# Optimization experiments

Measured on AMD Instinct MI355X. Metric: run time of the kernel, lower is better.

The kernel has to match this reference:

```python
import jax, jax.numpy as jnp
import numpy as np

EPS = 1e-06

def _l2_norm(t):
    # normalize over channel dim (-2): einsum('bcn,bn->bcn', t, 1/||t||_{2,dim=-2})
    inv = 1.0 / jnp.linalg.norm(t, ord=2, axis=-2)  # (B, L)
    return t * inv[:, None, :]


def setup_inputs() -> dict:
    key = jax.random.key(0)
    ks = jax.random.split(key, 8)
    B, C, D = 16, 2048, 1024  # D == d_model == Length
    s = 1.0 / np.sqrt(D)
    return {
        "x": jax.random.normal(ks[0], (B, C, D), dtype=jnp.float32),
        "Wq": jax.random.normal(ks[1], (D, D), dtype=jnp.float32) * s,
        "bq": jnp.zeros((D,), dtype=jnp.float32),
        "Wk": jax.random.normal(ks[2], (D, D), dtype=jnp.float32) * s,
        "bk": jnp.zeros((D,), dtype=jnp.float32),
        "Wv": jax.random.normal(ks[3], (D, D), dtype=jnp.float32) * s,
        "bv": jnp.zeros((D,), dtype=jnp.float32),
        "gamma": jax.random.normal(ks[4], (1,), dtype=jnp.float32) * 0.1,
    }


def reference(x, Wq, bq, Wk, bk, Wv, bv, gamma):
    B, C, L = x.shape
    # Linear layers act on last dim (torch Linear: x @ W.T + b)
    Q = x @ Wq.T + bq            # (B, C, L)
    K = x @ Wk.T + bk            # (B, C, L)
    V = x @ Wv.T + bv            # (B, C, L)
    Q = jnp.transpose(_l2_norm(Q), (0, 2, 1))  # (B, L, C)
    K = _l2_norm(K)                            # (B, C, L)
    # tailor_sum: (B, L)
    tailor_sum = 1.0 / (L + jnp.einsum('bnc,bc->bn', Q, jnp.sum(K, axis=-1) + EPS))
    # value_sum: (B, C) broadcast over L
    value_sum = jnp.sum(V, axis=-1)[:, :, None]            # (B, C, 1)
    matrix = jnp.einsum('bmn,bcn->bmc', K, V)              # (B, C, C)
    matrix_sum = value_sum + jnp.einsum('bnm,bmc->bcn', Q, matrix)  # (B, C, L)
    weight_value = matrix_sum * tailor_sum[:, None, :]     # (B, C, L)
    return x + gamma * weight_value
```

## Files before the change

### kernel.cpp

```cpp
#include <hip/hip_runtime.h>
#include <cstdint>

#define DEV static __device__ __forceinline__

typedef __attribute__((ext_vector_type(4))) float f32x4;
typedef __attribute__((ext_vector_type(4))) float fl4;
typedef __attribute__((ext_vector_type(4))) unsigned short us4;
typedef __attribute__((ext_vector_type(8))) unsigned short us8;
typedef __attribute__((ext_vector_type(2))) long l2v;

DEV float b2f(unsigned short u) {
  union { unsigned int i; float f; } c; c.i = ((unsigned int)u) << 16; return c.f;
}
DEV unsigned short f2b(float f) {
  union { float f; unsigned int i; } c; c.f = f;
  unsigned int u = c.i;
  u += 0x7fffu + ((u >> 16) & 1u);
  return (unsigned short)(u >> 16);
}
DEV unsigned int f4_to_fp8x4(float a, float b, float c, float d) {
  int r = __builtin_amdgcn_cvt_pk_fp8_f32(a, b, 0, false);
  r = __builtin_amdgcn_cvt_pk_fp8_f32(c, d, r, true);
  return (unsigned int)r;
}
DEV unsigned char f2f8(float v) {
  return (unsigned char)__builtin_amdgcn_cvt_pk_fp8_f32(v, v, 0, false);
}

DEV void gload16(const void* g, void* l) {
  __builtin_amdgcn_global_load_lds(
      (const __attribute__((address_space(1))) unsigned int*)g,
      (__attribute__((address_space(3))) unsigned int*)l, 16, 0, 0);
}

DEV float red16(float v) {
  v += __shfl_xor(v, 1); v += __shfl_xor(v, 2);
  v += __shfl_xor(v, 4); v += __shfl_xor(v, 8);
  return v;
}
DEV float red4lk(float v) {
  v += __shfl_xor(v, 16); v += __shfl_xor(v, 32);
  return v;
}

__global__ __launch_bounds__(256) void k_xcast(const float* __restrict__ src,
                                               unsigned short* __restrict__ dh,
                                               unsigned char* __restrict__ d8, long n) {
  long i = ((long)blockIdx.x * 256 + threadIdx.x) * 4;
  if (i >= n) return;
  fl4 v = *(const fl4*)(src + i);
  us4 o;
  o[0] = f2b(v[0]); o[1] = f2b(v[1]); o[2] = f2b(v[2]); o[3] = f2b(v[3]);
  *(us4*)(dh + i) = o;
  *(unsigned int*)(d8 + i) = f4_to_fp8x4(v[0], v[1], v[2], v[3]);
}

__global__ __launch_bounds__(256) void k_wcast8(const float* __restrict__ wq,
                                                const float* __restrict__ wk,
                                                const float* __restrict__ wv,
                                                unsigned char* __restrict__ dst) {
  const long i = ((long)blockIdx.x * 256 + threadIdx.x) * 4;
  const int seg = (int)(i >> 20);
  const float* s = seg == 0 ? wq : (seg == 1 ? wk : wv);
  fl4 v = *(const fl4*)(s + (i & 1048575));
  *(unsigned int*)(dst + i) = f4_to_fp8x4(v[0], v[1], v[2], v[3]);
}

__global__ __launch_bounds__(256) void k_bias_cat(const float* __restrict__ bq,
                                                  const float* __restrict__ bk,
                                                  const float* __restrict__ bv,
                                                  float* __restrict__ o) {
  const int t = blockIdx.x * 256 + threadIdx.x;
  o[t] = t < 1024 ? bq[t] : (t < 2048 ? bk[t - 1024] : bv[t - 2048]);
}

#define MFMA_FP8(A, B, C) __builtin_amdgcn_mfma_f32_16x16x32_fp8_fp8((A), (B), (C), 0, 0, 0)
#define SBAR   __builtin_amdgcn_s_barrier()

__global__ __launch_bounds__(512, 4)
void k_g8qkv8(const unsigned char* __restrict__ A,
              const unsigned char* __restrict__ Bt,
              unsigned char* __restrict__ QT8, unsigned char* __restrict__ KT8,
              unsigned char* __restrict__ Vout8,
              int Kb,
              const float* __restrict__ bias,
              float* __restrict__ r1, float* __restrict__ r2,
              float* __restrict__ r3, float* __restrict__ r4) {
  __shared__ __align__(16) unsigned char LDSU[73728];

  const int tid = threadIdx.x;
  const int wv = tid >> 6, lane = tid & 63;
  const int wr = wv >> 2, wcn = wv & 3;
  const int l15 = lane & 15, lk = lane >> 4;

  const int nx = gridDim.x;
  const int nwg = nx * gridDim.y;
  const int lin = blockIdx.y * nx + blockIdx.x;
  const int cpx = nwg >> 3;
  const int wg = (lin & 7) * cpx + (lin >> 3);
  const int bn = wg % nx;
  const int bm = wg / nx;

  const unsigned char* Ab = A + (long)bm * 128 * Kb;
  const unsigned char* Bb = Bt + (long)bn * 256 * Kb;

  const int scsw = (tid & 3) ^ ((tid >> 3) & 3);
  const long gOff = (long)(tid >> 2) * Kb + (long)scsw * 16;
  const int ldsb = wv * 1024;

  const int rdsw = (lk ^ ((l15 >> 1) & 3)) * 16;
  const int abase = (wr * 64 + l15) * 64;
  const int bbase = (wcn * 64 + l15) * 64;

  f32x4 acc[4][4];
#pragma unroll
  for (int i = 0; i < 4; ++i)
#pragma unroll
    for (int j = 0; j < 4; ++j) acc[i][j] = (f32x4){0.f, 0.f, 0.f, 0.f};

#define STAGEQ(T, BUF)                                                              \
  {                                                                                 \
    const long kb = (long)(T) * 64;                                                 \
    gload16(Ab + kb + gOff,             LDSU + (BUF) * 8192 + ldsb);                \
    gload16(Bb + kb + gOff,             LDSU + 24576 + (BUF) * 16384 + ldsb);       \
    gload16(Bb + kb + gOff + 128L * Kb, LDSU + 24576 + (BUF) * 16384 + 8192 + ldsb);\
  }

  STAGEQ(0, 0)
  STAGEQ(1, 1)

  const int NT = Kb >> 6;
  for (int t = 0; t < NT; ++t) {
    if (t < NT - 1) { asm volatile("s_waitcnt vmcnt(3)" ::: "memory"); }
    else            { asm volatile("s_waitcnt vmcnt(0)" ::: "memory"); }
    SBAR;
    if (t + 2 < NT) { STAGEQ(t + 2, (t + 2) % 3) }

    const unsigned char* Asc = LDSU + (t % 3) * 8192;
    const unsigned char* Bsc = LDSU + 24576 + (t % 3) * 16384;
    l2v Bf[4], Af[4];
#pragma unroll
    for (int j = 0; j < 4; ++j)
      Bf[j] = *(const l2v*)&Bsc[bbase + j * 1024 + rdsw];
#pragma unroll
    for (int i = 0; i < 4; ++i)
      Af[i] = *(const l2v*)&Asc[abase + i * 1024 + rdsw];

    __builtin_amdgcn_s_setprio(1);
#pragma unroll
    for (int i = 0; i < 4; ++i)
#pragma unroll
      for (int j = 0; j < 4; ++j) {
        acc[i][j] = MFMA_FP8(Af[i][0], Bf[j][0], acc[i][j]);
        acc[i][j] = MFMA_FP8(Af[i][1], Bf[j][1], acc[i][j]);
      }
    __builtin_amdgcn_s_setprio(0);
  }
#undef STAGEQ
  SBAR;

  const int col0 = bn * 256 + wcn * 64;
  const int seg = bn >> 2;
  const int b = bm >> 4;
  float bvj[4];
#pragma unroll
  for (int j = 0; j < 4; ++j) bvj[j] = bias[col0 + j * 16 + l15];
  const int colL0 = col0 & 1023;
  unsigned char* sc8 = LDSU;

  if (seg < 2) {
#pragma unroll
    for (int i = 0; i < 4; ++i)
#pragma unroll
      for (int j = 0; j < 4; ++j) {
        const int p = wcn * 64 + j * 16 + l15;
        const int m = wr * 64 + i * 16 + lk * 4;
        const unsigned int pk4 = f4_to_fp8x4(acc[i][j][0] + bvj[j], acc[i][j][1] + bvj[j],
                                             acc[i][j][2] + bvj[j], acc[i][j][3] + bvj[j]);
        *(unsigned int*)&sc8[p * 128 + (((m >> 4) ^ (p & 7)) << 4) + (m & 15)] = pk4;
      }
#pragma unroll
    for (int j = 0; j < 4; ++j) {
      const int colL = colL0 + j * 16 + l15;
      float ss = 0.f, sm = 0.f;
#pragma unroll
      for (int i = 0; i < 4; ++i)
#pragma unroll
        for (int r = 0; r < 4; ++r) {
          const float v = acc[i][j][r] + bvj[j];
          ss += v * v; sm += v;
        }
      ss = red4lk(ss);
      if (seg == 0) sm = red4lk(sm);
      if (lk == 0) {
        atomicAdd(&(seg == 0 ? r1 : r3)[(long)b * 1024 + colL], ss);
        if (seg == 0) atomicAdd(&r2[(long)b * 1024 + colL], sm);
      }
    }
    SBAR;
    unsigned char* tp = (seg == 0 ? QT8 : KT8) + (long)b * 2097152;
    const int P0 = (bn & 3) * 256;
    const int M0 = (bm & 15) * 128;
#pragma unroll
    for (int it = 0; it < 4; ++it) {
      const int p = it * 64 + (tid >> 3);
      const int c = tid & 7;
      us8 v = *(const us8*)&sc8[p * 128 + ((c ^ (p & 7)) << 4)];
      *(us8*)&tp[(long)(P0 + p) * 2048 + M0 + c * 16] = v;
    }
  } else {
#pragma unroll
    for (int i = 0; i < 4; ++i)
#pragma unroll
      for (int r = 0; r < 4; ++r) {
        const int rl = wr * 64 + i * 16 + lk * 4 + r;
        float sm = 0.f;
#pragma unroll
        for (int j = 0; j < 4; ++j) {
          const float v = acc[i][j][r] + bvj[j];
          sm += v;
          const int col = wcn * 64 + j * 16 + l15;
          sc8[rl * 256 + (((col >> 4) ^ (rl & 15)) << 4) + (col & 15)] = f2f8(v);
        }
        sm = red16(sm);
        if (l15 == 0) atomicAdd(&r4[bm * 128 + rl], sm);
      }
    SBAR;
    const int C0 = (bn & 3) * 256;
#pragma unroll
    for (int it = 0; it < 4; ++it) {
      const int rl = it * 32 + (tid >> 4);
      const int c = tid & 15;
      us8 v = *(const us8*)&sc8[rl * 256 + ((c ^ (rl & 15)) << 4)];
      *(us8*)&Vout8[(long)(bm * 128 + rl) * 1024 + C0 + c * 16] = v;
    }
  }
}

__global__ __launch_bounds__(1024, 4)
void k_g16s8(const unsigned char* __restrict__ A,
             const unsigned char* __restrict__ Bt,
             unsigned char* __restrict__ Sout,
             int Kb,
             const float* __restrict__ pq, const float* __restrict__ pk,
             float* __restrict__ Srow) {
  __shared__ __align__(16) unsigned char LDSU[131072];

  const int tid = threadIdx.x;
  const int wv = tid >> 6, lane = tid & 63;
  const int wr = wv >> 2, wcn = wv & 3;
  const int l15 = lane & 15, lk = lane >> 4;

  const int nx = gridDim.x;
  const int nwg = nx * gridDim.y;
  const int lin = blockIdx.y * nx + blockIdx.x;
  const int cpx = nwg >> 3;
  const int wg = (lin & 7) * cpx + (lin >> 3);
  const int bn = wg % nx;
  const int bm = wg / nx;
  const int bz = blockIdx.z;

  const unsigned char* Ab = A + (long)bz * 2097152 + (long)bm * 256 * Kb;
  const unsigned char* Bb = Bt + (long)bz * 2097152 + (long)bn * 256 * Kb;

  const int scsw = (tid & 3) ^ ((tid >> 3) & 3);
  const long gOff = (long)(tid >> 2) * Kb + (long)scsw * 16;
  const int ldsb = wv * 1024;

  const int rdsw = (lk ^ ((l15 >> 1) & 3)) * 16;
  const int abase = (wr * 64 + l15) * 64;
  const int bbase = (wcn * 64 + l15) * 64;

  f32x4 acc[4][4];
#pragma unroll
  for (int i = 0; i < 4; ++i)
#pragma unroll
    for (int j = 0; j < 4; ++j) acc[i][j] = (f32x4){0.f, 0.f, 0.f, 0.f};

#define STAGES(T, BUF)                                                        \
  {                                                                           \
    const long kb = (long)(T) * 64;                                           \
    gload16(Ab + kb + gOff, LDSU + (BUF) * 16384 + ldsb);                     \
    gload16(Bb + kb + gOff, LDSU + 65536 + (BUF) * 16384 + ldsb);             \
  }

  STAGES(0, 0)
  STAGES(1, 1)

  const int NT = Kb >> 6;
  for (int t = 0; t < NT; ++t) {
    if (t < NT - 1) { asm volatile("s_waitcnt vmcnt(2)" ::: "memory"); }
    else            { asm volatile("s_waitcnt vmcnt(0)" ::: "memory"); }
    if ((t & 1) == 0) SBAR;
    if (t + 2 < NT) STAGES(t + 2, (t + 2) & 3)

    const unsigned char* Asc = LDSU + (t & 3) * 16384;
    const unsigned char* Bsc = LDSU + 65536 + (t & 3) * 16384;
    l2v Bf[4], Af[4];
#pragma unroll
    for (int j = 0; j < 4; ++j)
      Bf[j] = *(const l2v*)&Bsc[bbase + j * 1024 + rdsw];
#pragma unroll
    for (int i = 0; i < 4; ++i)
      Af[i] = *(const l2v*)&Asc[abase + i * 1024 + rdsw];

    __builtin_amdgcn_s_setprio(1);
#pragma unroll
    for (int i = 0; i < 4; ++i)
#pragma unroll
      for (int j = 0; j < 4; ++j) {
        acc[i][j] = MFMA_FP8(Af[i][0], Bf[j][0], acc[i][j]);
        acc[i][j] = MFMA_FP8(Af[i][1], Bf[j][1], acc[i][j]);
      }
    __builtin_amdgcn_s_setprio(0);
  }
#undef STAGES
  SBAR;

  const int row0 = bm * 256 + wr * 64;
  const int col0 = bn * 256 + wcn * 64;
  unsigned char* sc8 = LDSU;

  float ivk[4];
#pragma unroll
  for (int j = 0; j < 4; ++j) ivk[j] = rsqrtf(pk[bz * 1024 + col0 + j * 16 + l15]);
#pragma unroll
  for (int i = 0; i < 4; ++i)
#pragma unroll
    for (int r = 0; r < 4; ++r) {
      const int rl = wr * 64 + i * 16 + lk * 4 + r;
      const float ivq = rsqrtf(pq[bz * 1024 + row0 + i * 16 + lk * 4 + r]);
      float sm = 0.f;
#pragma unroll
      for (int j = 0; j < 4; ++j) {
        const float v = acc[i][j][r] * ivq * ivk[j];
        sm += v;
        const int col = wcn * 64 + j * 16 + l15;
        sc8[rl * 256 + (((col >> 4) ^ (rl & 15)) << 4) + (col & 15)] = f2f8(v);
      }
      sm = red16(sm);
      if (l15 == 0) atomicAdd(&Srow[(long)bz * 1024 + row0 + i * 16 + lk * 4 + r], sm);
    }
  SBAR;
  unsigned char* Cb = Sout + (long)bz * 1048576;
#pragma unroll
  for (int it = 0; it < 4; ++it) {
    const int rl = it * 64 + (tid >> 4);
    const int c = tid & 15;
    us8 v = *(const us8*)&sc8[rl * 256 + ((c ^ (rl & 15)) << 4)];
    *(us8*)&Cb[(long)(bm * 256 + rl) * 1024 + bn * 256 + c * 16] = v;
  }
}

__global__ __launch_bounds__(1024, 4)
void k_g16fin(const unsigned char* __restrict__ A,
              const unsigned char* __restrict__ Bt,
              float* __restrict__ Out,
              int Kb,
              const unsigned short* __restrict__ xh,
              const float* __restrict__ Vsum,
              const float* __restrict__ Srow,
              const float* __restrict__ pq,
              const float* __restrict__ qsum,
              const float* __restrict__ gptr) {
  __shared__ __align__(16) unsigned char LDSU[131072];

  const int tid = threadIdx.x;
  const int wv = tid >> 6, lane = tid & 63;
  const int wr = wv >> 2, wcn = wv & 3;
  const int l15 = lane & 15, lk = lane >> 4;

  const int nx = gridDim.x;
  const int nwg = nx * gridDim.y;
  const int lin = blockIdx.y * nx + blockIdx.x;
  const int cpx = nwg >> 3;
  const int wg = (lin & 7) * cpx + (lin >> 3);
  const int bn = wg % nx;
  const int bm = wg / nx;
  const int bz = blockIdx.z;

  const unsigned char* Ab = A + (long)bz * 2097152 + (long)bm * 256 * Kb;
  const unsigned char* Bb = Bt + (long)bz * 1048576 + (long)bn * 256 * Kb;

  const int scsw = (tid & 3) ^ ((tid >> 3) & 3);
  const long gOff = (long)(tid >> 2) * Kb + (long)scsw * 16;
  const int ldsb = wv * 1024;

  const int rdsw = (lk ^ ((l15 >> 1) & 3)) * 16;
  const int abase = (wr * 64 + l15) * 64;
  const int bbase = (wcn * 64 + l15) * 64;

  f32x4 acc[4][4];
#pragma unroll
  for (int i = 0; i < 4; ++i)
#pragma unroll
    for (int j = 0; j < 4; ++j) acc[i][j] = (f32x4){0.f, 0.f, 0.f, 0.f};

#define STAGEF(T, BUF)                                                        \
  {                                                                           \
    const long kb = (long)(T) * 64;                                           \
    gload16(Ab + kb + gOff, LDSU + (BUF) * 16384 + ldsb);                     \
    gload16(Bb + kb + gOff, LDSU + 65536 + (BUF) * 16384 + ldsb);             \
  }

  STAGEF(0, 0)
  STAGEF(1, 1)

  const int NT = Kb >> 6;
  for (int t = 0; t < NT; ++t) {
    if (t < NT - 1) { asm volatile("s_waitcnt vmcnt(2)" ::: "memory"); }
    else            { asm volatile("s_waitcnt vmcnt(0)" ::: "memory"); }
    if ((t & 1) == 0) SBAR;
    if (t + 2 < NT) STAGEF(t + 2, (t + 2) & 3)

    const unsigned char* Asc = LDSU + (t & 3) * 16384;
    const unsigned char* Bsc = LDSU + 65536 + (t & 3) * 16384;
    l2v Bf[4], Af[4];
#pragma unroll
    for (int j = 0; j < 4; ++j)
      Bf[j] = *(const l2v*)&Bsc[bbase + j * 1024 + rdsw];
#pragma unroll
    for (int i = 0; i < 4; ++i)
      Af[i] = *(const l2v*)&Asc[abase + i * 1024 + rdsw];

    __builtin_amdgcn_s_setprio(1);
#pragma unroll
    for (int i = 0; i < 4; ++i)
#pragma unroll
      for (int j = 0; j < 4; ++j) {
        acc[i][j] = MFMA_FP8(Af[i][0], Bf[j][0], acc[i][j]);
        acc[i][j] = MFMA_FP8(Af[i][1], Bf[j][1], acc[i][j]);
      }
    __builtin_amdgcn_s_setprio(0);
  }
#undef STAGEF
  SBAR;

  float* scf = (float*)LDSU;
  float* Cb = Out + (long)bz * 2097152;
  const float g = gptr[0];
#pragma unroll
  for (int h = 0; h < 4; ++h) {
    if (wr == h) {
#pragma unroll
      for (int i = 0; i < 4; ++i)
#pragma unroll
        for (int j = 0; j < 4; ++j) {
          const int col = wcn * 64 + j * 16 + l15;
          const int cc = col >> 2, c3 = col & 3;
#pragma unroll
          for (int r = 0; r < 4; ++r) {
            const int rl = i * 16 + lk * 4 + r;
            scf[rl * 256 + ((cc ^ (rl & 15)) << 2) + c3] = acc[i][j][r];
          }
        }
    }
    SBAR;
#pragma unroll
    for (int it = 0; it < 4; ++it) {
      const int rl = it * 16 + wv;
      const int rg = bm * 256 + h * 64 + rl;
      const int c = lane;
      fl4 a4 = *(const fl4*)&scf[rl * 256 + ((c ^ (rl & 15)) << 2)];
      const int cg = bn * 256 + c * 4;
      us4 xv = *(const us4*)&xh[((long)bz * 2048 + rg) * 1024 + cg];
      fl4 sr = *(const fl4*)&Srow[bz * 1024 + cg];
      fl4 pq4 = *(const fl4*)&pq[bz * 1024 + cg];
      fl4 qs4 = *(const fl4*)&qsum[bz * 1024 + cg];
      const float vs = Vsum[bz * 2048 + rg];
      fl4 o;
#pragma unroll
      for (int q = 0; q < 4; ++q) {
        const float tl = 1.0f / (1024.0f + sr[q] + 1e-6f * rsqrtf(pq4[q]) * qs4[q]);
        o[q] = b2f(xv[q]) + g * ((vs + a4[q]) * tl);
      }
      *(fl4*)&Cb[(long)rg * 1024 + cg] = o;
    }
    if (h < 3) SBAR;
  }
}

extern "C" void kernel_launch(void* const* d_in, const int* in_sizes, int n_in,
                              void* d_out, int out_size, void* d_ws, size_t ws_size,
                              hipStream_t stream) {
  (void)in_sizes; (void)n_in; (void)out_size;
  const float* x     = (const float*)d_in[0];
  const float* Wq    = (const float*)d_in[1];
  const float* bq    = (const float*)d_in[2];
  const float* Wk    = (const float*)d_in[3];
  const float* bk    = (const float*)d_in[4];
  const float* Wv    = (const float*)d_in[5];
  const float* bv    = (const float*)d_in[6];
  const float* gamma = (const float*)d_in[7];

  const long NE = 16L * 2048 * 1024;

  char* w = (char*)d_ws;
  unsigned char*  QT8 = (unsigned char*)(w);
  unsigned char*  KT8 = (unsigned char*)(w + 33554432L);
  unsigned char*  V8  = (unsigned char*)(w + 67108864L);
  unsigned short* xh  = (unsigned short*)(w + 100663296L);
  unsigned char*  x8  = (unsigned char*)(w + 167772160L);
  unsigned char*  S8  = (unsigned char*)(w + 201326592L);
  size_t off = 218103808L;
  unsigned char* W8   = (unsigned char*)(w + off); off += 3145728;
  char* accbase = w + off;
  float* pq     = (float*)(w + off); off += 65536;
  float* qsum   = (float*)(w + off); off += 65536;
  float* pk     = (float*)(w + off); off += 65536;
  float* Vsum   = (float*)(w + off); off += 131072;
  float* Srow   = (float*)(w + off); off += 65536;
  const size_t accbytes = (size_t)(w + off - accbase);
  float* bqkv   = (float*)(w + off); off += 12288;
  if (ws_size < off) return;

  hipMemsetAsync(accbase, 0, accbytes, stream);

  k_xcast<<<dim3((unsigned)(NE / 1024)), 256, 0, stream>>>(x, xh, x8, NE);
  k_wcast8<<<dim3(3072), 256, 0, stream>>>(Wq, Wk, Wv, W8);
  k_bias_cat<<<dim3(12), 256, 0, stream>>>(bq, bk, bv, bqkv);

  k_g8qkv8<<<dim3(12, 256, 1), 512, 0, stream>>>(
      x8, W8, QT8, KT8, V8, 1024, bqkv, pq, qsum, pk, Vsum);

  k_g16s8<<<dim3(4, 4, 16), 1024, 0, stream>>>(
      QT8, KT8, S8, 2048, pq, pk, Srow);

  k_g16fin<<<dim3(4, 8, 16), 1024, 0, stream>>>(
      V8, S8, (float*)d_out, 1024, xh, Vsum, Srow, pq, qsum, gamma);
}
```

Baseline: 332.0 us.

## Shrink S and final GEMM tiles to 128x256 with 512-thread blocks

The second and third GEMMs (the per-batch S computation and the final output GEMM) move from 256x256 tiles with 1024-thread blocks to 128x256 tiles with 512-thread blocks. They now share the 3-stage K-loop and prologue already used by the QKV GEMM, and the grid doubles to 512 and 1024 workgroups. The goal is better occupancy and load balance on the CUs, plus smaller LDS use per block. The cost is less data reuse per tile, so more global and L2 traffic for the A and B operands.

```diff
diff --git a/kernel.cpp b/kernel.cpp
--- a/kernel.cpp
+++ b/kernel.cpp
@@ -77,6 +77,60 @@
 #define MFMA_FP8(A, B, C) __builtin_amdgcn_mfma_f32_16x16x32_fp8_fp8((A), (B), (C), 0, 0, 0)
 #define SBAR   __builtin_amdgcn_s_barrier()
 
+#define KLOOP8(STG)                                                            \
+  STG(0, 0)                                                                    \
+  STG(1, 1)                                                                    \
+  const int NT = Kb >> 6;                                                      \
+  for (int t = 0; t < NT; ++t) {                                               \
+    if (t < NT - 1) { asm volatile("s_waitcnt vmcnt(3)" ::: "memory"); }       \
+    else            { asm volatile("s_waitcnt vmcnt(0)" ::: "memory"); }       \
+    SBAR;                                                                      \
+    if (t + 2 < NT) { STG(t + 2, (t + 2) % 3) }                                \
+    const unsigned char* Asc = LDSU + (t % 3) * 8192;                          \
+    const unsigned char* Bsc = LDSU + 24576 + (t % 3) * 16384;                 \
+    l2v Bf[4], Af[4];                                                          \
+    _Pragma("unroll")                                                          \
+    for (int j = 0; j < 4; ++j)                                                \
+      Bf[j] = *(const l2v*)&Bsc[bbase + j * 1024 + rdsw];                      \
+    _Pragma("unroll")                                                          \
+    for (int i = 0; i < 4; ++i)                                                \
+      Af[i] = *(const l2v*)&Asc[abase + i * 1024 + rdsw];                      \
+    __builtin_amdgcn_s_setprio(1);                                             \
+    _Pragma("unroll")                                                          \
+    for (int i = 0; i < 4; ++i)                                                \
+      _Pragma("unroll")                                                        \
+      for (int j = 0; j < 4; ++j) {                                            \
+        acc[i][j] = MFMA_FP8(Af[i][0], Bf[j][0], acc[i][j]);                   \
+        acc[i][j] = MFMA_FP8(Af[i][1], Bf[j][1], acc[i][j]);                   \
+      }                                                                        \
+    __builtin_amdgcn_s_setprio(0);                                             \
+  }                                                                            \
+  SBAR;
+
+#define PROLOG8                                                                \
+  const int tid = threadIdx.x;                                                 \
+  const int wv = tid >> 6, lane = tid & 63;                                    \
+  const int wr = wv >> 2, wcn = wv & 3;                                        \
+  const int l15 = lane & 15, lk = lane >> 4;                                   \
+  const int nx = gridDim.x;                                                    \
+  const int nwg = nx * gridDim.y;                                              \
+  const int lin = blockIdx.y * nx + blockIdx.x;                                \
+  const int cpx = nwg >> 3;                                                    \
+  const int wg = (lin & 7) * cpx + (lin >> 3);                                 \
+  const int bn = wg % nx;                                                      \
+  const int bm = wg / nx;                                                      \
+  const int scsw = (tid & 3) ^ ((tid >> 3) & 3);                               \
+  const long gOff = (long)(tid >> 2) * Kb + (long)scsw * 16;                   \
+  const int ldsb = wv * 1024;                                                  \
+  const int rdsw = (lk ^ ((l15 >> 1) & 3)) * 16;                               \
+  const int abase = (wr * 64 + l15) * 64;                                      \
+  const int bbase = (wcn * 64 + l15) * 64;                                     \
+  f32x4 acc[4][4];                                                             \
+  _Pragma("unroll")                                                            \
+  for (int i = 0; i < 4; ++i)                                                  \
+    _Pragma("unroll")                                                          \
+    for (int j = 0; j < 4; ++j) acc[i][j] = (f32x4){0.f, 0.f, 0.f, 0.f};
+
 __global__ __launch_bounds__(512, 4)
 void k_g8qkv8(const unsigned char* __restrict__ A,
               const unsigned char* __restrict__ Bt,
@@ -87,36 +141,9 @@
               float* __restrict__ r1, float* __restrict__ r2,
               float* __restrict__ r3, float* __restrict__ r4) {
   __shared__ __align__(16) unsigned char LDSU[73728];
-
-  const int tid = threadIdx.x;
-  const int wv = tid >> 6, lane = tid & 63;
-  const int wr = wv >> 2, wcn = wv & 3;
-  const int l15 = lane & 15, lk = lane >> 4;
-
-  const int nx = gridDim.x;
-  const int nwg = nx * gridDim.y;
-  const int lin = blockIdx.y * nx + blockIdx.x;
-  const int cpx = nwg >> 3;
-  const int wg = (lin & 7) * cpx + (lin >> 3);
-  const int bn = wg % nx;
-  const int bm = wg / nx;
-
+  PROLOG8
   const unsigned char* Ab = A + (long)bm * 128 * Kb;
   const unsigned char* Bb = Bt + (long)bn * 256 * Kb;
-
-  const int scsw = (tid & 3) ^ ((tid >> 3) & 3);
-  const long gOff = (long)(tid >> 2) * Kb + (long)scsw * 16;
-  const int ldsb = wv * 1024;
-
-  const int rdsw = (lk ^ ((l15 >> 1) & 3)) * 16;
-  const int abase = (wr * 64 + l15) * 64;
-  const int bbase = (wcn * 64 + l15) * 64;
-
-  f32x4 acc[4][4];
-#pragma unroll
-  for (int i = 0; i < 4; ++i)
-#pragma unroll
-    for (int j = 0; j < 4; ++j) acc[i][j] = (f32x4){0.f, 0.f, 0.f, 0.f};
 
 #define STAGEQ(T, BUF)                                                              \
   {                                                                                 \
@@ -125,39 +152,8 @@
     gload16(Bb + kb + gOff,             LDSU + 24576 + (BUF) * 16384 + ldsb);       \
     gload16(Bb + kb + gOff + 128L * Kb, LDSU + 24576 + (BUF) * 16384 + 8192 + ldsb);\
   }
-
-  STAGEQ(0, 0)
-  STAGEQ(1, 1)
-
-  const int NT = Kb >> 6;
-  for (int t = 0; t < NT; ++t) {
-    if (t < NT - 1) { asm volatile("s_waitcnt vmcnt(3)" ::: "memory"); }
-    else            { asm volatile("s_waitcnt vmcnt(0)" ::: "memory"); }
-    SBAR;
-    if (t + 2 < NT) { STAGEQ(t + 2, (t + 2) % 3) }
-
-    const unsigned char* Asc = LDSU + (t % 3) * 8192;
-    const unsigned char* Bsc = LDSU + 24576 + (t % 3) * 16384;
-    l2v Bf[4], Af[4];
-#pragma unroll
-    for (int j = 0; j < 4; ++j)
-      Bf[j] = *(const l2v*)&Bsc[bbase + j * 1024 + rdsw];
-#pragma unroll
-    for (int i = 0; i < 4; ++i)
-      Af[i] = *(const l2v*)&Asc[abase + i * 1024 + rdsw];
-
-    __builtin_amdgcn_s_setprio(1);
-#pragma unroll
-    for (int i = 0; i < 4; ++i)
-#pragma unroll
-      for (int j = 0; j < 4; ++j) {
-        acc[i][j] = MFMA_FP8(Af[i][0], Bf[j][0], acc[i][j]);
-        acc[i][j] = MFMA_FP8(Af[i][1], Bf[j][1], acc[i][j]);
-      }
-    __builtin_amdgcn_s_setprio(0);
-  }
+  KLOOP8(STAGEQ)
 #undef STAGEQ
-  SBAR;
 
   const int col0 = bn * 256 + wcn * 64;
   const int seg = bn >> 2;
@@ -237,87 +233,29 @@
   }
 }
 
-__global__ __launch_bounds__(1024, 4)
-void k_g16s8(const unsigned char* __restrict__ A,
-             const unsigned char* __restrict__ Bt,
-             unsigned char* __restrict__ Sout,
-             int Kb,
-             const float* __restrict__ pq, const float* __restrict__ pk,
-             float* __restrict__ Srow) {
-  __shared__ __align__(16) unsigned char LDSU[131072];
-
-  const int tid = threadIdx.x;
-  const int wv = tid >> 6, lane = tid & 63;
-  const int wr = wv >> 2, wcn = wv & 3;
-  const int l15 = lane & 15, lk = lane >> 4;
-
-  const int nx = gridDim.x;
-  const int nwg = nx * gridDim.y;
-  const int lin = blockIdx.y * nx + blockIdx.x;
-  const int cpx = nwg >> 3;
-  const int wg = (lin & 7) * cpx + (lin >> 3);
-  const int bn = wg % nx;
-  const int bm = wg / nx;
+__global__ __launch_bounds__(512, 4)
+void k_g8s8(const unsigned char* __restrict__ A,
+            const unsigned char* __restrict__ Bt,
+            unsigned char* __restrict__ Sout,
+            int Kb,
+            const float* __restrict__ pq, const float* __restrict__ pk,
+            float* __restrict__ Srow) {
+  __shared__ __align__(16) unsigned char LDSU[73728];
+  PROLOG8
   const int bz = blockIdx.z;
-
-  const unsigned char* Ab = A + (long)bz * 2097152 + (long)bm * 256 * Kb;
+  const unsigned char* Ab = A + (long)bz * 2097152 + (long)bm * 128 * Kb;
   const unsigned char* Bb = Bt + (long)bz * 2097152 + (long)bn * 256 * Kb;
 
-  const int scsw = (tid & 3) ^ ((tid >> 3) & 3);
-  const long gOff = (long)(tid >> 2) * Kb + (long)scsw * 16;
-  const int ldsb = wv * 1024;
-
-  const int rdsw = (lk ^ ((l15 >> 1) & 3)) * 16;
-  const int abase = (wr * 64 + l15) * 64;
-  const int bbase = (wcn * 64 + l15) * 64;
-
-  f32x4 acc[4][4];
-#pragma unroll
-  for (int i = 0; i < 4; ++i)
-#pragma unroll
-    for (int j = 0; j < 4; ++j) acc[i][j] = (f32x4){0.f, 0.f, 0.f, 0.f};
-
-#define STAGES(T, BUF)                                                        \
-  {                                                                           \
-    const long kb = (long)(T) * 64;                                           \
-    gload16(Ab + kb + gOff, LDSU + (BUF) * 16384 + ldsb);                     \
-    gload16(Bb + kb + gOff, LDSU + 65536 + (BUF) * 16384 + ldsb);             \
-  }
-
-  STAGES(0, 0)
-  STAGES(1, 1)
-
-  const int NT = Kb >> 6;
-  for (int t = 0; t < NT; ++t) {
-    if (t < NT - 1) { asm volatile("s_waitcnt vmcnt(2)" ::: "memory"); }
-    else            { asm volatile("s_waitcnt vmcnt(0)" ::: "memory"); }
-    if ((t & 1) == 0) SBAR;
-    if (t + 2 < NT) STAGES(t + 2, (t + 2) & 3)
-
-    const unsigned char* Asc = LDSU + (t & 3) * 16384;
-    const unsigned char* Bsc = LDSU + 65536 + (t & 3) * 16384;
-    l2v Bf[4], Af[4];
-#pragma unroll
-    for (int j = 0; j < 4; ++j)
-      Bf[j] = *(const l2v*)&Bsc[bbase + j * 1024 + rdsw];
-#pragma unroll
-    for (int i = 0; i < 4; ++i)
-      Af[i] = *(const l2v*)&Asc[abase + i * 1024 + rdsw];
-
-    __builtin_amdgcn_s_setprio(1);
-#pragma unroll
-    for (int i = 0; i < 4; ++i)
-#pragma unroll
-      for (int j = 0; j < 4; ++j) {
-        acc[i][j] = MFMA_FP8(Af[i][0], Bf[j][0], acc[i][j]);
-        acc[i][j] = MFMA_FP8(Af[i][1], Bf[j][1], acc[i][j]);
-      }
-    __builtin_amdgcn_s_setprio(0);
-  }
+#define STAGES(T, BUF)                                                              \
+  {                                                                                 \
+    const long kb = (long)(T) * 64;                                                 \
+    gload16(Ab + kb + gOff,             LDSU + (BUF) * 8192 + ldsb);                \
+    gload16(Bb + kb + gOff,             LDSU + 24576 + (BUF) * 16384 + ldsb);       \
+    gload16(Bb + kb + gOff + 128L * Kb, LDSU + 24576 + (BUF) * 16384 + 8192 + ldsb);\
+  }
+  KLOOP8(STAGES)
 #undef STAGES
-  SBAR;
-
-  const int row0 = bm * 256 + wr * 64;
+
   const int col0 = bn * 256 + wcn * 64;
   unsigned char* sc8 = LDSU;
 
@@ -329,7 +267,8 @@
 #pragma unroll
     for (int r = 0; r < 4; ++r) {
       const int rl = wr * 64 + i * 16 + lk * 4 + r;
-      const float ivq = rsqrtf(pq[bz * 1024 + row0 + i * 16 + lk * 4 + r]);
+      const int rowg = bm * 128 + rl;
+      const float ivq = rsqrtf(pq[bz * 1024 + rowg]);
       float sm = 0.f;
 #pragma unroll
       for (int j = 0; j < 4; ++j) {
@@ -339,108 +278,52 @@
         sc8[rl * 256 + (((col >> 4) ^ (rl & 15)) << 4) + (col & 15)] = f2f8(v);
       }
       sm = red16(sm);
-      if (l15 == 0) atomicAdd(&Srow[(long)bz * 1024 + row0 + i * 16 + lk * 4 + r], sm);
+      if (l15 == 0) atomicAdd(&Srow[(long)bz * 1024 + rowg], sm);
     }
   SBAR;
   unsigned char* Cb = Sout + (long)bz * 1048576;
+  const int C0 = bn * 256;
 #pragma unroll
   for (int it = 0; it < 4; ++it) {
-    const int rl = it * 64 + (tid >> 4);
+    const int rl = it * 32 + (tid >> 4);
     const int c = tid & 15;
     us8 v = *(const us8*)&sc8[rl * 256 + ((c ^ (rl & 15)) << 4)];
-    *(us8*)&Cb[(long)(bm * 256 + rl) * 1024 + bn * 256 + c * 16] = v;
-  }
-}
-
-__global__ __launch_bounds__(1024, 4)
-void k_g16fin(const unsigned char* __restrict__ A,
-              const unsigned char* __restrict__ Bt,
-              float* __restrict__ Out,
-              int Kb,
-              const unsigned short* __restrict__ xh,
-              const float* __restrict__ Vsum,
-              const float* __restrict__ Srow,
-              const float* __restrict__ pq,
-              const float* __restrict__ qsum,
-              const float* __restrict__ gptr) {
-  __shared__ __align__(16) unsigned char LDSU[131072];
-
-  const int tid = threadIdx.x;
-  const int wv = tid >> 6, lane = tid & 63;
-  const int wr = wv >> 2, wcn = wv & 3;
-  const int l15 = lane & 15, lk = lane >> 4;
-
-  const int nx = gridDim.x;
-  const int nwg = nx * gridDim.y;
-  const int lin = blockIdx.y * nx + blockIdx.x;
-  const int cpx = nwg >> 3;
-  const int wg = (lin & 7) * cpx + (lin >> 3);
-  const int bn = wg % nx;
-  const int bm = wg / nx;
+    *(us8*)&Cb[(long)(bm * 128 + rl) * 1024 + C0 + c * 16] = v;
+  }
+}
+
+__global__ __launch_bounds__(512, 4)
+void k_g8fin(const unsigned char* __restrict__ A,
+             const unsigned char* __restrict__ Bt,
+             float* __restrict__ Out,
+             int Kb,
+             const unsigned short* __restrict__ xh,
+             const float* __restrict__ Vsum,
+             const float* __restrict__ Srow,
+             const float* __restrict__ pq,
+             const float* __restrict__ qsum,
+             const float* __restrict__ gptr) {
+  __shared__ __align__(16) unsigned char LDSU[73728];
+  PROLOG8
   const int bz = blockIdx.z;
-
-  const unsigned char* Ab = A + (long)bz * 2097152 + (long)bm * 256 * Kb;
+  const unsigned char* Ab = A + (long)bz * 2097152 + (long)bm * 128 * Kb;
   const unsigned char* Bb = Bt + (long)bz * 1048576 + (long)bn * 256 * Kb;
 
-  const int scsw = (tid & 3) ^ ((tid >> 3) & 3);
-  const long gOff = (long)(tid >> 2) * Kb + (long)scsw * 16;
-  const int ldsb = wv * 1024;
-
-  const int rdsw = (lk ^ ((l15 >> 1) & 3)) * 16;
-  const int abase = (wr * 64 + l15) * 64;
-  const int bbase = (wcn * 64 + l15) * 64;
-
-  f32x4 acc[4][4];
-#pragma unroll
-  for (int i = 0; i < 4; ++i)
-#pragma unroll
-    for (int j = 0; j < 4; ++j) acc[i][j] = (f32x4){0.f, 0.f, 0.f, 0.f};
-
-#define STAGEF(T, BUF)                                                        \
-  {                                                                           \
-    const long kb = (long)(T) * 64;                                           \
-    gload16(Ab + kb + gOff, LDSU + (BUF) * 16384 + ldsb);                     \
-    gload16(Bb + kb + gOff, LDSU + 65536 + (BUF) * 16384 + ldsb);             \
-  }
-
-  STAGEF(0, 0)
-  STAGEF(1, 1)
-
-  const int NT = Kb >> 6;
-  for (int t = 0; t < NT; ++t) {
-    if (t < NT - 1) { asm volatile("s_waitcnt vmcnt(2)" ::: "memory"); }
-    else            { asm volatile("s_waitcnt vmcnt(0)" ::: "memory"); }
-    if ((t & 1) == 0) SBAR;
-    if (t + 2 < NT) STAGEF(t + 2, (t + 2) & 3)
-
-    const unsigned char* Asc = LDSU + (t & 3) * 16384;
-    const unsigned char* Bsc = LDSU + 65536 + (t & 3) * 16384;
-    l2v Bf[4], Af[4];
-#pragma unroll
-    for (int j = 0; j < 4; ++j)
-      Bf[j] = *(const l2v*)&Bsc[bbase + j * 1024 + rdsw];
-#pragma unroll
-    for (int i = 0; i < 4; ++i)
-      Af[i] = *(const l2v*)&Asc[abase + i * 1024 + rdsw];
-
-    __builtin_amdgcn_s_setprio(1);
-#pragma unroll
-    for (int i = 0; i < 4; ++i)
-#pragma unroll
-      for (int j = 0; j < 4; ++j) {
-        acc[i][j] = MFMA_FP8(Af[i][0], Bf[j][0], acc[i][j]);
-        acc[i][j] = MFMA_FP8(Af[i][1], Bf[j][1], acc[i][j]);
-      }
-    __builtin_amdgcn_s_setprio(0);
-  }
+#define STAGEF(T, BUF)                                                              \
+  {                                                                                 \
+    const long kb = (long)(T) * 64;                                                 \
+    gload16(Ab + kb + gOff,             LDSU + (BUF) * 8192 + ldsb);                \
+    gload16(Bb + kb + gOff,             LDSU + 24576 + (BUF) * 16384 + ldsb);       \
+    gload16(Bb + kb + gOff + 128L * Kb, LDSU + 24576 + (BUF) * 16384 + 8192 + ldsb);\
+  }
+  KLOOP8(STAGEF)
 #undef STAGEF
-  SBAR;
 
   float* scf = (float*)LDSU;
   float* Cb = Out + (long)bz * 2097152;
   const float g = gptr[0];
 #pragma unroll
-  for (int h = 0; h < 4; ++h) {
+  for (int h = 0; h < 2; ++h) {
     if (wr == h) {
 #pragma unroll
       for (int i = 0; i < 4; ++i)
@@ -457,9 +340,9 @@
     }
     SBAR;
 #pragma unroll
-    for (int it = 0; it < 4; ++it) {
-      const int rl = it * 16 + wv;
-      const int rg = bm * 256 + h * 64 + rl;
+    for (int it = 0; it < 8; ++it) {
+      const int rl = it * 8 + wv;
+      const int rg = bm * 128 + h * 64 + rl;
       const int c = lane;
       fl4 a4 = *(const fl4*)&scf[rl * 256 + ((c ^ (rl & 15)) << 2)];
       const int cg = bn * 256 + c * 4;
@@ -476,7 +359,7 @@
       }
       *(fl4*)&Cb[(long)rg * 1024 + cg] = o;
     }
-    if (h < 3) SBAR;
+    if (h == 0) SBAR;
   }
 }
 
@@ -523,9 +406,9 @@
   k_g8qkv8<<<dim3(12, 256, 1), 512, 0, stream>>>(
       x8, W8, QT8, KT8, V8, 1024, bqkv, pq, qsum, pk, Vsum);
 
-  k_g16s8<<<dim3(4, 4, 16), 1024, 0, stream>>>(
+  k_g8s8<<<dim3(4, 8, 16), 512, 0, stream>>>(
       QT8, KT8, S8, 2048, pq, pk, Srow);
 
-  k_g16fin<<<dim3(4, 8, 16), 1024, 0, stream>>>(
+  k_g8fin<<<dim3(4, 16, 16), 512, 0, stream>>>(
       V8, S8, (float*)d_out, 1024, xh, Vsum, Srow, pq, qsum, gamma);
 }
```

Result: slower. 339.7 us (+2.3%).
